# Kernel tuning notes

Hardware: AMD Instinct MI355X
Metric: run time of the kernel (lower is better)

Reference implementation:

```python
import jax, jax.numpy as jnp
import numpy as np

NEG_SLOPE = 0.2
BN_EPS = 1e-5


def _gat_conv(x, src, dst, W, a_src, a_dst, b, n_nodes):
    # PyG GATConv, heads=1: linear, per-edge leaky-relu score, per-dst softmax, scatter-add.
    h = x @ W  # [N, C]
    e = jax.nn.leaky_relu((h @ a_src)[src] + (h @ a_dst)[dst], NEG_SLOPE)  # [E]
    m = jax.ops.segment_max(e, dst, num_segments=n_nodes)
    m = jnp.where(jnp.isfinite(m), m, 0.0)  # nodes with no in-edges
    w = jnp.exp(e - m[dst])
    denom = jax.ops.segment_sum(w, dst, num_segments=n_nodes)
    alpha = w / (denom[dst] + 1e-16)  # [E]
    out = jax.ops.segment_sum(alpha[:, None] * h[src], dst, num_segments=n_nodes)
    return out + b


def setup_inputs() -> dict:
    key = jax.random.key(0)
    N, E, Q, C = 50000, 800000, 200000, 128
    ks = jax.random.split(key, 12)
    sc = 1.0 / np.sqrt(C)
    d = {
        "embedding": jax.random.normal(ks[0], (N, C), jnp.float32) * 0.1,
        "W1": jax.random.normal(ks[1], (C, C), jnp.float32) * sc,
        "a_src1": jax.random.normal(ks[2], (C,), jnp.float32) * sc,
        "a_dst1": jax.random.normal(ks[3], (C,), jnp.float32) * sc,
        "b1": jnp.zeros((C,), jnp.float32),
        "gamma": jnp.ones((C,), jnp.float32),
        "beta": jnp.zeros((C,), jnp.float32),
        "rmean": jnp.zeros((C,), jnp.float32),
        "rvar": jnp.ones((C,), jnp.float32),
        "W2": jax.random.normal(ks[4], (C, C), jnp.float32) * sc,
        "a_src2": jax.random.normal(ks[5], (C,), jnp.float32) * sc,
        "a_dst2": jax.random.normal(ks[6], (C,), jnp.float32) * sc,
        "b2": jnp.zeros((C,), jnp.float32),
        "Wp1": jax.random.normal(ks[7], (C, C), jnp.float32) * sc,
        "bp1": jnp.zeros((C,), jnp.float32),
        "Wp2": jax.random.normal(ks[8], (C, 1), jnp.float32) * sc,
        "bp2": jnp.zeros((1,), jnp.float32),
        "edge_index": jax.random.randint(ks[9], (2, E), 0, N, jnp.int32),
        "edges": jax.random.randint(ks[10], (2, Q), 0, N, jnp.int32),
    }
    return d


def reference(embedding, W1, a_src1, a_dst1, b1, gamma, beta, rmean, rvar,
              W2, a_src2, a_dst2, b2, Wp1, bp1, Wp2, bp2, edge_index, edges):
    N = embedding.shape[0]
    src, dst = edge_index[0], edge_index[1]
    # conv0 -> BN (eval, running stats) -> ReLU (dropout inactive in eval)
    x = _gat_conv(embedding, src, dst, W1, a_src1, a_dst1, b1, N)
    x = (x - rmean) * jax.lax.rsqrt(rvar + BN_EPS) * gamma + beta
    x = jax.nn.relu(x)
    # final conv
    x = _gat_conv(x, src, dst, W2, a_src2, a_dst2, b2, N)
    # LinkPredictor: elementwise product of endpoint embeddings -> MLP -> sigmoid
    h = x[edges[0]] * x[edges[1]]  # [Q, C]
    h = jax.nn.relu(h @ Wp1 + bp1)
    out = jax.nn.sigmoid(h @ Wp2 + bp2)
    return out[:, 0]
```

## Files before the change

kernel.cpp:

```cpp
#include <hip/hip_runtime.h>
#include <hip/hip_bf16.h>
#include <math.h>
#include <stdint.h>
#include <string.h>

#define NEG_SLOPE 0.2f
#define BN_EPS 1e-5f

typedef __attribute__((ext_vector_type(8))) short short8;
typedef __attribute__((ext_vector_type(4))) float float4v;

static __device__ __forceinline__ unsigned short f2bf(float f) {
    union { float f; unsigned u; } v; v.f = f;
    unsigned r = (v.u + 0x7fffu + ((v.u >> 16) & 1u)) >> 16;
    return (unsigned short)r;
}
static __device__ __forceinline__ float bf2f(unsigned short u) {
    union { unsigned u; float f; } v; v.u = ((unsigned)u) << 16;
    return v.f;
}

__global__ __launch_bounds__(128) void bn_prep(const float* __restrict__ gamma,
                                               const float* __restrict__ beta,
                                               const float* __restrict__ rmean,
                                               const float* __restrict__ rvar,
                                               float* __restrict__ scale,
                                               float* __restrict__ shift) {
    int c = threadIdx.x;
    float s = gamma[c] * rsqrtf(rvar[c] + BN_EPS);
    scale[c] = s;
    shift[c] = beta[c] - rmean[c] * s;
}

__global__ __launch_bounds__(256) void w_to_bf16T(const float* __restrict__ W,
                                                  unsigned short* __restrict__ WT) {
    int idx = blockIdx.x * 256 + threadIdx.x;
    int k = idx >> 7, n = idx & 127;
    WT[n * 128 + k] = f2bf(W[idx]);
}

#define BK_CAP 8192
#define BK_EPB 4096

__global__ __launch_bounds__(256) void bucket_scatter(const int* __restrict__ src,
                                                      const int* __restrict__ dst,
                                                      int* __restrict__ bcur,
                                                      unsigned long long* __restrict__ bucket,
                                                      int E) {
    __shared__ int lcnt[256];
    __shared__ int lbase[256];
    int t = threadIdx.x;
    int e0 = blockIdx.x * BK_EPB;
    lcnt[t] = 0;
    __syncthreads();

    int es[16], ed[16];
#pragma unroll
    for (int u = 0; u < 16; ++u) {
        int i = e0 + u * 256 + t;
        if (i < E) {
            es[u] = src[i];
            ed[u] = dst[i];
            atomicAdd(&lcnt[ed[u] >> 8], 1);
        } else {
            ed[u] = -1;
        }
    }
    __syncthreads();
    int c = lcnt[t];
    if (c > 0) lbase[t] = atomicAdd(&bcur[t], c);
    __syncthreads();
    lcnt[t] = 0;
    __syncthreads();
#pragma unroll
    for (int u = 0; u < 16; ++u) {
        if (ed[u] >= 0) {
            int bin = ed[u] >> 8;
            int r = atomicAdd(&lcnt[bin], 1);
            int slot = lbase[bin] + r;
            if (slot < BK_CAP)
                bucket[(size_t)bin * BK_CAP + slot] =
                    ((unsigned long long)(ed[u] & 255) << 32) | (unsigned)es[u];
        }
    }
}

__global__ __launch_bounds__(256) void bucket_deg(const int* __restrict__ bcur,
                                                  const unsigned long long* __restrict__ bucket,
                                                  int* __restrict__ deg, int N) {
    __shared__ int cnt[256];
    int t = threadIdx.x, b = blockIdx.x;
    cnt[t] = 0;
    __syncthreads();
    int c = bcur[b];
    if (c > BK_CAP) c = BK_CAP;
    for (int i = t; i < c; i += 256)
        atomicAdd(&cnt[(int)(bucket[(size_t)b * BK_CAP + i] >> 32)], 1);
    __syncthreads();
    int node = (b << 8) + t;
    if (node < N) deg[node] = cnt[t];
}

__global__ __launch_bounds__(256) void scan_block_reduce(const int* __restrict__ deg,
                                                         int* __restrict__ bsum, int N) {
    __shared__ int s[256];
    int t = threadIdx.x;
    int i = blockIdx.x * 256 + t;
    s[t] = (i < N) ? deg[i] : 0;
    __syncthreads();
#pragma unroll
    for (int d = 128; d; d >>= 1) {
        if (t < d) s[t] += s[t + d];
        __syncthreads();
    }
    if (t == 0) bsum[blockIdx.x] = s[0];
}

__global__ __launch_bounds__(1024) void scan_block_sums(int* __restrict__ bsum,
                                                        int* __restrict__ offs,
                                                        int nb, int N) {
    __shared__ int s[1024];
    int t = threadIdx.x;
    int v = (t < nb) ? bsum[t] : 0;
    s[t] = v;
    __syncthreads();
    for (int d = 1; d < 1024; d <<= 1) {
        int u = (t >= d) ? s[t - d] : 0;
        __syncthreads();
        s[t] += u;
        __syncthreads();
    }
    if (t < nb) bsum[t] = s[t] - v;
    if (t == 1023) offs[N] = s[1023];
}

__global__ __launch_bounds__(256) void scan_write_offsets(const int* __restrict__ deg,
                                                          const int* __restrict__ bsum,
                                                          int* __restrict__ offs, int N) {
    __shared__ int s[256];
    int t = threadIdx.x;
    int i = blockIdx.x * 256 + t;
    int v = (i < N) ? deg[i] : 0;
    s[t] = v;
    __syncthreads();
    for (int d = 1; d < 256; d <<= 1) {
        int u = (t >= d) ? s[t - d] : 0;
        __syncthreads();
        s[t] += u;
        __syncthreads();
    }
    if (i < N) offs[i] = bsum[blockIdx.x] + s[t] - v;
}

__global__ __launch_bounds__(256) void bucket_fill(const int* __restrict__ bcur,
                                                   const unsigned long long* __restrict__ bucket,
                                                   const int* __restrict__ offs,
                                                   int* __restrict__ csr, int N) {
    __shared__ int cur[256];
    int t = threadIdx.x;
    int b = blockIdx.x;
    int base_node = b << 8;
    int node = base_node + t;
    cur[t] = (node < N) ? offs[node] : 0;
    __syncthreads();
    int cnt = bcur[b];
    if (cnt > BK_CAP) cnt = BK_CAP;
    for (int i = t; i < cnt; i += 256) {
        unsigned long long v = bucket[(size_t)b * BK_CAP + i];
        int dl = (int)(v >> 32);
        int s = (int)(v & 0xffffffffu);
        int r = atomicAdd(&cur[dl], 1);
        csr[r] = s;
    }
}

#define LP_RS 136

template <bool BF16_IN>
__global__ __launch_bounds__(256) void gemm_mfma(
    const void* __restrict__ Xv,
    const unsigned short* __restrict__ WT,
    const float* __restrict__ a_src, const float* __restrict__ a_dst,
    unsigned short* __restrict__ H,
    float* __restrict__ s_src, float* __restrict__ s_dst, int N)
{
    __shared__ unsigned short sA[128 * LP_RS];
    __shared__ unsigned short sW[128 * LP_RS];
    const float* Xf = (const float*)Xv;
    const unsigned short* Xh = (const unsigned short*)Xv;
    int tid = threadIdx.x;
    int r0 = blockIdx.x * 128;

#pragma unroll
    for (int it = 0; it < 8; ++it) {
        int idx = it * 2048 + tid * 8;
        int n = idx >> 7, k = idx & 127;
        *(short8*)&sW[n * LP_RS + k] = *(const short8*)&WT[idx];
    }
#pragma unroll
    for (int it = 0; it < 16; ++it) {
        int r = it * 8 + (tid >> 5);
        int c = (tid & 31) * 4;
        int row = r0 + r;
        ushort4 u = make_ushort4(0, 0, 0, 0);
        if (row < N) {
            if (BF16_IN) {
                u = *(const ushort4*)&Xh[(size_t)row * 128 + c];
            } else {
                float4 x = *(const float4*)&Xf[(size_t)row * 128 + c];
                u.x = f2bf(x.x); u.y = f2bf(x.y); u.z = f2bf(x.z); u.w = f2bf(x.w);
            }
        }
        *(ushort4*)&sA[r * LP_RS + c] = u;
    }
    __syncthreads();

    int wave = tid >> 6, lane = tid & 63;
    int ln = lane & 15, quad = lane >> 4;
    int rowbase = wave * 32;

    short8 af[2][4];
#pragma unroll
    for (int m = 0; m < 2; ++m)
#pragma unroll
        for (int kt = 0; kt < 4; ++kt)
            af[m][kt] = *(const short8*)&sA[(rowbase + m * 16 + ln) * LP_RS + kt * 32 + quad * 8];

    float4v acc[2][8];
#pragma unroll
    for (int m = 0; m < 2; ++m)
#pragma unroll
        for (int n = 0; n < 8; ++n)
            acc[m][n] = float4v{0.f, 0.f, 0.f, 0.f};

#pragma unroll
    for (int n = 0; n < 8; ++n) {
#pragma unroll
        for (int kt = 0; kt < 4; ++kt) {
            short8 bf = *(const short8*)&sW[(n * 16 + ln) * LP_RS + kt * 32 + quad * 8];
            acc[0][n] = __builtin_amdgcn_mfma_f32_16x16x32_bf16(af[0][kt], bf, acc[0][n], 0, 0, 0);
            acc[1][n] = __builtin_amdgcn_mfma_f32_16x16x32_bf16(af[1][kt], bf, acc[1][n], 0, 0, 0);
        }
    }

    float asr[8], adr[8];
#pragma unroll
    for (int n = 0; n < 8; ++n) {
        asr[n] = a_src[n * 16 + ln];
        adr[n] = a_dst[n * 16 + ln];
    }
#pragma unroll
    for (int m = 0; m < 2; ++m) {
        int rb = r0 + rowbase + m * 16 + quad * 4;
#pragma unroll
        for (int n = 0; n < 8; ++n) {
            int col = n * 16 + ln;
            float4v a = acc[m][n];
            if (rb + 0 < N) H[(size_t)(rb + 0) * 128 + col] = f2bf(a[0]);
            if (rb + 1 < N) H[(size_t)(rb + 1) * 128 + col] = f2bf(a[1]);
            if (rb + 2 < N) H[(size_t)(rb + 2) * 128 + col] = f2bf(a[2]);
            if (rb + 3 < N) H[(size_t)(rb + 3) * 128 + col] = f2bf(a[3]);
        }
#pragma unroll
        for (int r = 0; r < 4; ++r) {
            float ps = 0.f, pd = 0.f;
#pragma unroll
            for (int n = 0; n < 8; ++n) {
                float v = acc[m][n][r];
                ps = fmaf(v, asr[n], ps);
                pd = fmaf(v, adr[n], pd);
            }
#pragma unroll
            for (int o = 1; o < 16; o <<= 1) {
                ps += __shfl_xor(ps, o);
                pd += __shfl_xor(pd, o);
            }
            int row = rb + r;
            if (ln == 0 && row < N) { s_src[row] = ps; s_dst[row] = pd; }
        }
    }
}

__global__ __launch_bounds__(256) void edge_softmax(const int* __restrict__ off,
                                                    const int* __restrict__ csr,
                                                    const float* __restrict__ s_src,
                                                    const float* __restrict__ s_dst,
                                                    float* __restrict__ we,
                                                    float* __restrict__ invd, int N) {
    int tid = threadIdx.x;
    int node = blockIdx.x * 16 + (tid >> 4);
    if (node >= N) return;
    int ln = tid & 15;
    int beg = off[node], end = off[node + 1];
    float sd = s_dst[node];

    float sw = 0.f;
    for (int i = beg + ln; i < end; i += 16) {
        float e = s_src[csr[i]] + sd;
        e = (e >= 0.f) ? e : NEG_SLOPE * e;
        float w = expf(e);
        we[i] = w;
        sw += w;
    }
#pragma unroll
    for (int o = 8; o; o >>= 1) sw += __shfl_xor(sw, o);
    if (ln == 0) invd[node] = 1.f / (sw + 1e-16f);
}

__global__ __launch_bounds__(256) void gat_gather(const unsigned short* __restrict__ H,
                                                  const int* __restrict__ off,
                                                  const int* __restrict__ csr,
                                                  const float* __restrict__ we,
                                                  const float* __restrict__ invd,
                                                  const float* __restrict__ bias,
                                                  const float* __restrict__ bn_scale,
                                                  const float* __restrict__ bn_shift,
                                                  int do_bn_relu,
                                                  unsigned short* __restrict__ out, int N) {
    int wave = threadIdx.x >> 6, lane = threadIdx.x & 63;
    int half = lane >> 5, hl = lane & 31;
    int node = blockIdx.x * 8 + wave * 2 + half;
    if (node >= N) return;
    int c0 = hl * 4;
    int beg = off[node], end = off[node + 1];
    float inv = invd[node];

    float a0 = 0.f, a1 = 0.f, a2 = 0.f, a3 = 0.f;
    int i = beg;
    for (; i + 8 <= end; i += 8) {
        int s[8]; float w[8]; ushort4 hv[8];
#pragma unroll
        for (int u = 0; u < 8; ++u) { s[u] = csr[i + u]; w[u] = we[i + u]; }
#pragma unroll
        for (int u = 0; u < 8; ++u)
            hv[u] = *(const ushort4*)&H[(size_t)s[u] * 128 + c0];
#pragma unroll
        for (int u = 0; u < 8; ++u) {
            a0 = fmaf(w[u], bf2f(hv[u].x), a0);
            a1 = fmaf(w[u], bf2f(hv[u].y), a1);
            a2 = fmaf(w[u], bf2f(hv[u].z), a2);
            a3 = fmaf(w[u], bf2f(hv[u].w), a3);
        }
    }
    for (; i < end; ++i) {
        int s = csr[i];
        float w = we[i];
        ushort4 hv = *(const ushort4*)&H[(size_t)s * 128 + c0];
        a0 = fmaf(w, bf2f(hv.x), a0);
        a1 = fmaf(w, bf2f(hv.y), a1);
        a2 = fmaf(w, bf2f(hv.z), a2);
        a3 = fmaf(w, bf2f(hv.w), a3);
    }
    float o0 = a0 * inv + bias[c0 + 0];
    float o1 = a1 * inv + bias[c0 + 1];
    float o2 = a2 * inv + bias[c0 + 2];
    float o3 = a3 * inv + bias[c0 + 3];
    if (do_bn_relu) {
        o0 = fmaxf(o0 * bn_scale[c0 + 0] + bn_shift[c0 + 0], 0.f);
        o1 = fmaxf(o1 * bn_scale[c0 + 1] + bn_shift[c0 + 1], 0.f);
        o2 = fmaxf(o2 * bn_scale[c0 + 2] + bn_shift[c0 + 2], 0.f);
        o3 = fmaxf(o3 * bn_scale[c0 + 3] + bn_shift[c0 + 3], 0.f);
    }
    ushort4 ov;
    ov.x = f2bf(o0); ov.y = f2bf(o1); ov.z = f2bf(o2); ov.w = f2bf(o3);
    *(ushort4*)&out[(size_t)node * 128 + c0] = ov;
}

__global__ __launch_bounds__(256) void link_pred_mfma(
    const unsigned short* __restrict__ X,
    const int* __restrict__ E0, const int* __restrict__ E1,
    const unsigned short* __restrict__ WTg,
    const float* __restrict__ bp1,
    const float* __restrict__ Wp2,
    const float* __restrict__ bp2_p,
    float* __restrict__ out, int Q)
{
    __shared__ unsigned short sW[128 * LP_RS];
    int tid = threadIdx.x;
    int wave = tid >> 6, lane = tid & 63;
    int ln = lane & 15, quad = lane >> 4;

    int tile = blockIdx.x * 4 + wave;
    int qbase = tile * 32;

    int ea[2], eb[2];
#pragma unroll
    for (int m = 0; m < 2; ++m) {
        int q = qbase + m * 16 + ln;
        if (q >= Q) q = Q - 1;
        ea[m] = E0[q];
        eb[m] = E1[q];
    }

#pragma unroll
    for (int it = 0; it < 8; ++it) {
        int idx = it * 2048 + tid * 8;
        int n = idx >> 7, k = idx & 127;
        *(short8*)&sW[n * LP_RS + k] = *(const short8*)&WTg[idx];
    }

    short8 ra[2][4], rb[2][4];
#pragma unroll
    for (int m = 0; m < 2; ++m) {
        const unsigned short* pa = &X[(size_t)ea[m] * 128 + quad * 8];
        const unsigned short* pb = &X[(size_t)eb[m] * 128 + quad * 8];
#pragma unroll
        for (int kt = 0; kt < 4; ++kt) {
            ra[m][kt] = *(const short8*)(pa + kt * 32);
            rb[m][kt] = *(const short8*)(pb + kt * 32);
        }
    }

    float bias[8], w2c[8];
#pragma unroll
    for (int n = 0; n < 8; ++n) {
        bias[n] = bp1[n * 16 + ln];
        w2c[n] = Wp2[n * 16 + ln];
    }
    float b2 = bp2_p[0];

    __syncthreads();

    short8 af[2][4];
#pragma unroll
    for (int m = 0; m < 2; ++m) {
#pragma unroll
        for (int kt = 0; kt < 4; ++kt) {
            short8 p;
#pragma unroll
            for (int j = 0; j < 8; j += 2) {
                float p0 = bf2f((unsigned short)ra[m][kt][j]) *
                           bf2f((unsigned short)rb[m][kt][j]);
                float p1 = bf2f((unsigned short)ra[m][kt][j + 1]) *
                           bf2f((unsigned short)rb[m][kt][j + 1]);
                __hip_bfloat162 h2 = __float22bfloat162_rn(make_float2(p0, p1));
                unsigned pr;
                memcpy(&pr, &h2, 4);
                p[j]     = (short)(pr & 0xffffu);
                p[j + 1] = (short)(pr >> 16);
            }
            af[m][kt] = p;
        }
    }

    float r0[2] = {0.f, 0.f}, r1[2] = {0.f, 0.f}, r2[2] = {0.f, 0.f}, r3[2] = {0.f, 0.f};
#pragma unroll
    for (int n = 0; n < 8; ++n) {
        float4v a0 = float4v{bias[n], bias[n], bias[n], bias[n]};
        float4v a1 = a0;
#pragma unroll
        for (int kt = 0; kt < 4; ++kt) {
            short8 bf = *(const short8*)&sW[(n * 16 + ln) * LP_RS + kt * 32 + quad * 8];
            a0 = __builtin_amdgcn_mfma_f32_16x16x32_bf16(af[0][kt], bf, a0, 0, 0, 0);
            a1 = __builtin_amdgcn_mfma_f32_16x16x32_bf16(af[1][kt], bf, a1, 0, 0, 0);
        }
        float w = w2c[n];
        r0[0] += fmaxf(a0[0], 0.f) * w;  r0[1] += fmaxf(a1[0], 0.f) * w;
        r1[0] += fmaxf(a0[1], 0.f) * w;  r1[1] += fmaxf(a1[1], 0.f) * w;
        r2[0] += fmaxf(a0[2], 0.f) * w;  r2[1] += fmaxf(a1[2], 0.f) * w;
        r3[0] += fmaxf(a0[3], 0.f) * w;  r3[1] += fmaxf(a1[3], 0.f) * w;
    }
#pragma unroll
    for (int m = 0; m < 2; ++m) {
#pragma unroll
        for (int o = 1; o < 16; o <<= 1) {
            r0[m] += __shfl_xor(r0[m], o);
            r1[m] += __shfl_xor(r1[m], o);
            r2[m] += __shfl_xor(r2[m], o);
            r3[m] += __shfl_xor(r3[m], o);
        }
        if (ln == 0) {
            int rbase = qbase + m * 16 + quad * 4;
            float rv[4] = {r0[m], r1[m], r2[m], r3[m]};
#pragma unroll
            for (int r = 0; r < 4; ++r) {
                int q = rbase + r;
                if (q < Q) out[q] = 1.f / (1.f + expf(-(rv[r] + b2)));
            }
        }
    }
}

extern "C" void kernel_launch(void* const* d_in, const int* in_sizes, int n_in,
                              void* d_out, int out_size, void* d_ws, size_t ws_size,
                              hipStream_t stream) {
    const float* emb    = (const float*)d_in[0];
    const float* W1     = (const float*)d_in[1];
    const float* a_src1 = (const float*)d_in[2];
    const float* a_dst1 = (const float*)d_in[3];
    const float* b1     = (const float*)d_in[4];
    const float* gamma  = (const float*)d_in[5];
    const float* beta   = (const float*)d_in[6];
    const float* rmean  = (const float*)d_in[7];
    const float* rvar   = (const float*)d_in[8];
    const float* W2     = (const float*)d_in[9];
    const float* a_src2 = (const float*)d_in[10];
    const float* a_dst2 = (const float*)d_in[11];
    const float* b2     = (const float*)d_in[12];
    const float* Wp1    = (const float*)d_in[13];
    const float* bp1    = (const float*)d_in[14];
    const float* Wp2    = (const float*)d_in[15];
    const float* bp2    = (const float*)d_in[16];
    const int* edge_index = (const int*)d_in[17];
    const int* edges      = (const int*)d_in[18];

    const int N = in_sizes[0] / 128;
    const int E = in_sizes[17] / 2;
    const int Q = in_sizes[18] / 2;
    const int* src = edge_index;
    const int* dst = edge_index + E;
    const int* e0 = edges;
    const int* e1 = edges + Q;
    float* out = (float*)d_out;

    uintptr_t base = (uintptr_t)d_ws;
    size_t cur = 0;
    auto take = [&](size_t bytes) -> void* {
        void* p = (void*)(base + cur);
        cur += (bytes + 255) & ~(size_t)255;
        return p;
    };
    unsigned short* bufA = (unsigned short*)take((size_t)N * 128 * 2);
    unsigned short* bufB = (unsigned short*)take((size_t)N * 128 * 2);
    float* s_src  = (float*)take((size_t)N * 4);
    float* s_dst  = (float*)take((size_t)N * 4);
    float* bnsc   = (float*)take(128 * 4);
    float* bnsh   = (float*)take(128 * 4);
    int*   deg    = (int*)take((size_t)N * 4);
    int*   offs   = (int*)take((size_t)(N + 1) * 4);
    int*   csr    = (int*)take((size_t)E * 4);
    float* we     = (float*)take((size_t)E * 4);
    float* invd   = (float*)take((size_t)N * 4);
    unsigned short* wt1 = (unsigned short*)take(128 * 128 * 2);
    unsigned short* wt2 = (unsigned short*)take(128 * 128 * 2);
    unsigned short* wtp = (unsigned short*)take(128 * 128 * 2);
    int nb = (N + 255) / 256;
    int*   bsum   = (int*)take((size_t)nb * 4);
    int*   bcur   = (int*)take((size_t)nb * 4);
    unsigned long long* bucket =
        (unsigned long long*)take((size_t)nb * BK_CAP * 8);
    (void)ws_size; (void)n_in; (void)out_size;

    hipMemsetAsync(bcur, 0, (size_t)nb * 4, stream);

    bn_prep<<<1, 128, 0, stream>>>(gamma, beta, rmean, rvar, bnsc, bnsh);
    w_to_bf16T<<<64, 256, 0, stream>>>(W1, wt1);
    w_to_bf16T<<<64, 256, 0, stream>>>(W2, wt2);
    w_to_bf16T<<<64, 256, 0, stream>>>(Wp1, wtp);

    bucket_scatter<<<(E + BK_EPB - 1) / BK_EPB, 256, 0, stream>>>(src, dst, bcur, bucket, E);
    bucket_deg<<<nb, 256, 0, stream>>>(bcur, bucket, deg, N);
    scan_block_reduce<<<nb, 256, 0, stream>>>(deg, bsum, N);
    scan_block_sums<<<1, 1024, 0, stream>>>(bsum, offs, nb, N);
    scan_write_offsets<<<nb, 256, 0, stream>>>(deg, bsum, offs, N);
    bucket_fill<<<nb, 256, 0, stream>>>(bcur, bucket, offs, csr, N);

    int gblk = (N + 127) / 128;
    gemm_mfma<false><<<gblk, 256, 0, stream>>>(emb, wt1, a_src1, a_dst1, bufA, s_src, s_dst, N);
    edge_softmax<<<(N + 15) / 16, 256, 0, stream>>>(offs, csr, s_src, s_dst, we, invd, N);
    gat_gather<<<(N + 7) / 8, 256, 0, stream>>>(bufA, offs, csr, we, invd, b1,
                                                bnsc, bnsh, 1, bufB, N);
    gemm_mfma<true><<<gblk, 256, 0, stream>>>(bufB, wt2, a_src2, a_dst2, bufA, s_src, s_dst, N);
    edge_softmax<<<(N + 15) / 16, 256, 0, stream>>>(offs, csr, s_src, s_dst, we, invd, N);
    gat_gather<<<(N + 7) / 8, 256, 0, stream>>>(bufA, offs, csr, we, invd, b2,
                                                nullptr, nullptr, 0, bufB, N);
    int ntiles = (Q + 31) / 32;
    int lblk = (ntiles + 3) / 4;
    link_pred_mfma<<<lblk, 256, 0, stream>>>(bufB, e0, e1, wtp, bp1, Wp2, bp2, out, Q);
}
```

Before: 284.0 us.

## Merge prep kernels and derive CSR offsets directly from bucket counts

```diff
diff --git a/kernel.cpp b/kernel.cpp
--- a/kernel.cpp
+++ b/kernel.cpp
@@ -20,23 +20,27 @@
     return v.f;
 }
 
-__global__ __launch_bounds__(128) void bn_prep(const float* __restrict__ gamma,
-                                               const float* __restrict__ beta,
-                                               const float* __restrict__ rmean,
-                                               const float* __restrict__ rvar,
-                                               float* __restrict__ scale,
-                                               float* __restrict__ shift) {
-    int c = threadIdx.x;
-    float s = gamma[c] * rsqrtf(rvar[c] + BN_EPS);
-    scale[c] = s;
-    shift[c] = beta[c] - rmean[c] * s;
-}
-
-__global__ __launch_bounds__(256) void w_to_bf16T(const float* __restrict__ W,
-                                                  unsigned short* __restrict__ WT) {
-    int idx = blockIdx.x * 256 + threadIdx.x;
-    int k = idx >> 7, n = idx & 127;
-    WT[n * 128 + k] = f2bf(W[idx]);
+__global__ __launch_bounds__(256) void prep_all(
+    const float* __restrict__ W1, const float* __restrict__ W2,
+    const float* __restrict__ Wp1,
+    unsigned short* __restrict__ wt1, unsigned short* __restrict__ wt2,
+    unsigned short* __restrict__ wtp,
+    const float* __restrict__ gamma, const float* __restrict__ beta,
+    const float* __restrict__ rmean, const float* __restrict__ rvar,
+    float* __restrict__ bnsc, float* __restrict__ bnsh) {
+    int b = blockIdx.x;
+    if (b < 192) {
+        const float* W = (b < 64) ? W1 : (b < 128) ? W2 : Wp1;
+        unsigned short* WT = (b < 64) ? wt1 : (b < 128) ? wt2 : wtp;
+        int idx = (b & 63) * 256 + threadIdx.x;
+        int k = idx >> 7, n = idx & 127;
+        WT[n * 128 + k] = f2bf(W[idx]);
+    } else if (threadIdx.x < 128) {
+        int c = threadIdx.x;
+        float s = gamma[c] * rsqrtf(rvar[c] + BN_EPS);
+        bnsc[c] = s;
+        bnsh[c] = beta[c] - rmean[c] * s;
+    }
 }
 
 #define BK_CAP 8192
@@ -85,43 +89,14 @@
     }
 }
 
-__global__ __launch_bounds__(256) void bucket_deg(const int* __restrict__ bcur,
-                                                  const unsigned long long* __restrict__ bucket,
-                                                  int* __restrict__ deg, int N) {
-    __shared__ int cnt[256];
-    int t = threadIdx.x, b = blockIdx.x;
-    cnt[t] = 0;
-    __syncthreads();
-    int c = bcur[b];
-    if (c > BK_CAP) c = BK_CAP;
-    for (int i = t; i < c; i += 256)
-        atomicAdd(&cnt[(int)(bucket[(size_t)b * BK_CAP + i] >> 32)], 1);
-    __syncthreads();
-    int node = (b << 8) + t;
-    if (node < N) deg[node] = cnt[t];
-}
-
-__global__ __launch_bounds__(256) void scan_block_reduce(const int* __restrict__ deg,
-                                                         int* __restrict__ bsum, int N) {
-    __shared__ int s[256];
-    int t = threadIdx.x;
-    int i = blockIdx.x * 256 + t;
-    s[t] = (i < N) ? deg[i] : 0;
-    __syncthreads();
-#pragma unroll
-    for (int d = 128; d; d >>= 1) {
-        if (t < d) s[t] += s[t + d];
-        __syncthreads();
-    }
-    if (t == 0) bsum[blockIdx.x] = s[0];
-}
-
-__global__ __launch_bounds__(1024) void scan_block_sums(int* __restrict__ bsum,
-                                                        int* __restrict__ offs,
-                                                        int nb, int N) {
+__global__ __launch_bounds__(1024) void scan_bucket_sums(const int* __restrict__ bcur,
+                                                         int* __restrict__ bbase,
+                                                         int* __restrict__ offs,
+                                                         int nb, int N) {
     __shared__ int s[1024];
     int t = threadIdx.x;
-    int v = (t < nb) ? bsum[t] : 0;
+    int v = 0;
+    if (t < nb) { v = bcur[t]; if (v > BK_CAP) v = BK_CAP; }
     s[t] = v;
     __syncthreads();
     for (int d = 1; d < 1024; d <<= 1) {
@@ -130,26 +105,35 @@
         s[t] += u;
         __syncthreads();
     }
-    if (t < nb) bsum[t] = s[t] - v;
+    if (t < nb) bbase[t] = s[t] - v;
     if (t == 1023) offs[N] = s[1023];
 }
 
-__global__ __launch_bounds__(256) void scan_write_offsets(const int* __restrict__ deg,
-                                                          const int* __restrict__ bsum,
-                                                          int* __restrict__ offs, int N) {
-    __shared__ int s[256];
-    int t = threadIdx.x;
-    int i = blockIdx.x * 256 + t;
-    int v = (i < N) ? deg[i] : 0;
-    s[t] = v;
+__global__ __launch_bounds__(256) void bucket_offs(const int* __restrict__ bcur,
+                                                   const unsigned long long* __restrict__ bucket,
+                                                   const int* __restrict__ bbase,
+                                                   int* __restrict__ offs, int N) {
+    __shared__ int cnt[256];
+    __shared__ int sc[256];
+    int t = threadIdx.x, b = blockIdx.x;
+    cnt[t] = 0;
+    __syncthreads();
+    int c = bcur[b];
+    if (c > BK_CAP) c = BK_CAP;
+    for (int i = t; i < c; i += 256)
+        atomicAdd(&cnt[(int)(bucket[(size_t)b * BK_CAP + i] >> 32)], 1);
+    __syncthreads();
+    int v = cnt[t];
+    sc[t] = v;
     __syncthreads();
     for (int d = 1; d < 256; d <<= 1) {
-        int u = (t >= d) ? s[t - d] : 0;
+        int u = (t >= d) ? sc[t - d] : 0;
         __syncthreads();
-        s[t] += u;
+        sc[t] += u;
         __syncthreads();
     }
-    if (i < N) offs[i] = bsum[blockIdx.x] + s[t] - v;
+    int node = (b << 8) + t;
+    if (node < N) offs[node] = bbase[b] + sc[t] - v;
 }
 
 __global__ __launch_bounds__(256) void bucket_fill(const int* __restrict__ bcur,
@@ -526,7 +510,6 @@
     float* s_dst  = (float*)take((size_t)N * 4);
     float* bnsc   = (float*)take(128 * 4);
     float* bnsh   = (float*)take(128 * 4);
-    int*   deg    = (int*)take((size_t)N * 4);
     int*   offs   = (int*)take((size_t)(N + 1) * 4);
     int*   csr    = (int*)take((size_t)E * 4);
     float* we     = (float*)take((size_t)E * 4);
@@ -535,24 +518,20 @@
     unsigned short* wt2 = (unsigned short*)take(128 * 128 * 2);
     unsigned short* wtp = (unsigned short*)take(128 * 128 * 2);
     int nb = (N + 255) / 256;
-    int*   bsum   = (int*)take((size_t)nb * 4);
     int*   bcur   = (int*)take((size_t)nb * 4);
+    int*   bbase  = (int*)take((size_t)nb * 4);
     unsigned long long* bucket =
         (unsigned long long*)take((size_t)nb * BK_CAP * 8);
     (void)ws_size; (void)n_in; (void)out_size;
 
     hipMemsetAsync(bcur, 0, (size_t)nb * 4, stream);
 
-    bn_prep<<<1, 128, 0, stream>>>(gamma, beta, rmean, rvar, bnsc, bnsh);
-    w_to_bf16T<<<64, 256, 0, stream>>>(W1, wt1);
-    w_to_bf16T<<<64, 256, 0, stream>>>(W2, wt2);
-    w_to_bf16T<<<64, 256, 0, stream>>>(Wp1, wtp);
+    prep_all<<<193, 256, 0, stream>>>(W1, W2, Wp1, wt1, wt2, wtp,
+                                      gamma, beta, rmean, rvar, bnsc, bnsh);
 
     bucket_scatter<<<(E + BK_EPB - 1) / BK_EPB, 256, 0, stream>>>(src, dst, bcur, bucket, E);
-    bucket_deg<<<nb, 256, 0, stream>>>(bcur, bucket, deg, N);
-    scan_block_reduce<<<nb, 256, 0, stream>>>(deg, bsum, N);
-    scan_block_sums<<<1, 1024, 0, stream>>>(bsum, offs, nb, N);
-    scan_write_offsets<<<nb, 256, 0, stream>>>(deg, bsum, offs, N);
+    scan_bucket_sums<<<1, 1024, 0, stream>>>(bcur, bbase, offs, nb, N);
+    bucket_offs<<<nb, 256, 0, stream>>>(bcur, bucket, bbase, offs, N);
     bucket_fill<<<nb, 256, 0, stream>>>(bcur, bucket, offs, csr, N);
 
     int gblk = (N + 127) / 128;
```

New measurement: 273.1 us. 3.8% less time.
